# Optimization experiments

Measured on AMD Instinct MI355X. Metric: run time of the kernel, lower is better.

The kernel has to match this reference:

```python
import jax, jax.numpy as jnp
import numpy as np

# Model constants matching init_kwargs
C1, C2, FS, IMG = 1024, 3, 16, 128
NF = FS * FS                     # n_features = 256 (== pos_out_dim)
L = C1 // NF                     # 4 hypernetwork-generated layers
WD = NF + (L - 1) * NF + L       # weight_dim = 1028
M = NF // 4                      # 64 frequencies per coord dim
SIGMA = 10.0
B = 8


def _coords_pe(b):
    """get_coords([IMG, IMG]) + positional_encoding, flattened to [b, IMG*IMG, NF]."""
    v0, v1 = -0.99999, 1.0
    r = (v1 - v0) / (2 * IMG)
    seq = v0 + r + 2 * r * jnp.arange(IMG, dtype=jnp.float32)
    gy, gx = jnp.meshgrid(seq, seq, indexing='ij')
    coords = jnp.stack([gy, gx], axis=-1)                 # [IMG, IMG, 2]
    j = jnp.arange(M, dtype=jnp.float32)
    coeffs = 2.0 * jnp.pi * (SIGMA ** (j / M))            # [M]
    vp = coeffs * coords[..., None]                       # [IMG, IMG, 2, M]
    pe = jnp.concatenate([jnp.cos(vp), jnp.sin(vp)], -1)  # [IMG, IMG, 2, 2M]
    pe = pe.reshape(IMG, IMG, 4 * M)                      # flatten(-2,-1)
    x2 = pe.reshape(1, IMG * IMG, NF)
    return jnp.broadcast_to(x2, (b, IMG * IMG, NF))


def setup_inputs() -> dict:
    key = jax.random.key(0)
    ks = jax.random.split(key, 5)
    std = 0.001  # matches _initialize_weights
    x = jax.random.normal(ks[0], (B, C1, FS, FS), jnp.float32)
    conv_w = std * jax.random.normal(ks[1], (C1 + L, C1), jnp.float32)  # 1x1 conv kernel
    conv_b = jnp.zeros((C1 + L,), jnp.float32)
    wfine_w = std * jax.random.normal(ks[2], (NF, NF), jnp.float32)
    wfine_b = jnp.zeros((NF,), jnp.float32)
    last1_w = std * jax.random.normal(ks[3], (C2, NF), jnp.float32)
    last1_b = jnp.zeros((C2,), jnp.float32)
    prelu_a = jnp.array(0.25, jnp.float32)  # nn.PReLU default single param
    return {"x": x, "conv_w": conv_w, "conv_b": conv_b,
            "wfine_w": wfine_w, "wfine_b": wfine_b,
            "last1_w": last1_w, "last1_b": last1_b, "prelu_a": prelu_a}


def reference(x, conv_w, conv_b, wfine_w, wfine_b, last1_w, last1_b, prelu_a):
    b = x.shape[0]
    x2 = _coords_pe(b)  # [b, N_px, NF]
    # 1x1 conv == channel matmul
    x1 = jnp.einsum('bchw,oc->bohw', x, conv_w) + conv_b[None, :, None, None]
    W = x1.reshape(b, WD, NF)
    W = jnp.einsum('bik,jk->bij', W, wfine_w) + wfine_b  # W_fine linear
    out = x2
    for j in range(L):
        wj = W[:, NF * j + j: NF * (j + 1) + j, :]           # [b, NF, NF]
        bj = W[:, NF * (j + 1) + j: NF * (j + 1) + j + 1, :]  # [b, 1, NF]
        h = jnp.einsum('bij,bjk->bik', out, wj) + bj
        out = jnp.where(h >= 0, h, prelu_a * h)              # PReLU
    out = jnp.einsum('bik,ck->bic', out, last1_w) + last1_b  # last1
    out = jax.nn.silu(out)                                   # SiLU
    out = out.transpose(0, 2, 1).reshape(b, C2, IMG, IMG)
    return out
```

## Files before the change

kernel.cpp:

```cpp
#include <hip/hip_runtime.h>
#include <hip/hip_fp16.h>
#include <math.h>

typedef _Float16 f16;
typedef _Float16 f16x4 __attribute__((ext_vector_type(4)));
typedef _Float16 f16x8 __attribute__((ext_vector_type(8)));
typedef float f32x4 __attribute__((ext_vector_type(4)));

#define MFMA16(a, b, c) __builtin_amdgcn_mfma_f32_16x16x32_f16((a), (b), (c), 0, 0, 0)

static constexpr float SW_W    = 1024.f;
static constexpr float SA_A    = 64.f;
static constexpr float INV_SW  = 1.f / 1024.f;
static constexpr float INV_SW2 = 1.f / (1024.f * 1024.f);
static constexpr float INV_SASW = 1.f / (64.f * 1024.f);

static constexpr size_t OFF_CY = 0;
static constexpr size_t OFF_CX = OFF_CY + 65536;
static constexpr size_t OFF_LW = OFF_CX + 65536;
static constexpr size_t OFF_S  = OFF_LW + 8192;
static constexpr size_t OFF_CW = OFF_S  + 1024;
static constexpr size_t OFF_WF = OFF_CW + (size_t)1088 * 1024 * 2;
static constexpr size_t OFF_M2 = OFF_WF + 131072;
static constexpr size_t OFF_W  = OFF_M2 + (size_t)8 * 256 * 1024 * 2;
static constexpr size_t OFF_AY = OFF_W  + (size_t)8 * 1028 * 256 * 4;
static constexpr size_t OFF_BX = OFF_AY + (size_t)8 * 128 * 256 * 2;
static constexpr size_t OFF_WT = OFF_BX + (size_t)8 * 128 * 256 * 2;

static __device__ inline f32x4 zero4() { f32x4 v = {0.f, 0.f, 0.f, 0.f}; return v; }

__global__ void k_prep(float* __restrict__ cy, float* __restrict__ cx,
                       f16* __restrict__ lwf, const float* __restrict__ lw,
                       const float* __restrict__ cw, f16* __restrict__ cw16,
                       const float* __restrict__ wf, f16* __restrict__ wf16,
                       float* __restrict__ S)
{
    const int bid = blockIdx.x;
    const int t = threadIdx.x;
    if (bid < 130) {
        int id = bid * 256 + t;
        const float r = 1.99999f / 256.f;
        if (id < 32768) {
            float* dst = (id < 16384) ? cy : cx;
            int e = id & 16383;
            int row = e >> 7, f = e & 127;
            float s = -0.99999f + r + 2.f * r * (float)row;
            float coef = 6.283185307179586f * powf(10.f, (float)(f & 63) * (1.f / 64.f));
            float arg = coef * s;
            dst[e] = (f < 64) ? cosf(arg) : sinf(arg);
        } else {
            int id2 = id - 32768;
            int c = id2 >> 6, lane = id2 & 63;
            int nlo = lane & 15, q4 = lane >> 4;
            f16x8 v;
            #pragma unroll
            for (int ko = 0; ko < 8; ko++)
                v[ko] = (nlo < 3) ? (f16)(lw[nlo * 256 + (c << 5) + (q4 << 3) + ko] * SW_W) : (f16)0.f;
            *(f16x8*)(lwf + id2 * 8) = v;
        }
        return;
    }
    if (bid < 674) {
        const int g8 = (bid - 130) * 256 + t;
        const int row = g8 >> 7, col0 = (g8 & 127) << 3;
        f16x8 v;
        if (row < 1028) {
            const float* src = cw + (size_t)row * 1024 + col0;
            #pragma unroll
            for (int i = 0; i < 8; i++) v[i] = (f16)(src[i] * SW_W);
        } else {
            #pragma unroll
            for (int i = 0; i < 8; i++) v[i] = (f16)0.f;
        }
        *(f16x8*)(cw16 + (size_t)g8 * 8) = v;
        return;
    }
    if (bid < 706) {
        const int gg = (bid - 674) * 256 + t;
        const int row = gg >> 5, col0 = (gg & 31) << 3;
        const float* src = wf + (size_t)row * 256 + col0;
        f16x8 v;
        #pragma unroll
        for (int i = 0; i < 8; i++) v[i] = (f16)(src[i] * SW_W);
        *(f16x8*)(wf16 + (size_t)gg * 8) = v;
        return;
    }
    {
        const float* src = wf + (size_t)t * 256;
        float s = 0.f;
        for (int k = 0; k < 256; k++) s += src[k];
        S[t] = s;
    }
}

__global__ __launch_bounds__(256, 4) void k_gemmA(
    const float* __restrict__ x, const f16* __restrict__ wf16,
    f16* __restrict__ M2)
{
    __shared__ __align__(16) f16 Ab[2][64 * 32];
    __shared__ __align__(16) f16 Bb[2][64 * 32];
    const int t = threadIdx.x;
    const int lane = t & 63;
    const int wc = t >> 6;
    const int nlo = lane & 15, q4 = lane >> 4;
    const int blk = blockIdx.x;
    const int b = blk >> 6, rem = blk & 63;
    const int jt = rem >> 4, ct = rem & 15;
    const int j0 = jt << 6, c0 = ct << 6;

    auto stageA = [&](int buf, int k0) {
        const float* src = x + (((size_t)((b << 10) + c0 + (t >> 2))) << 8) + k0 + ((t & 3) << 3);
        f16x8 v;
        #pragma unroll
        for (int i = 0; i < 8; i++) v[i] = (f16)src[i];
        *(f16x8*)(&Ab[buf][t << 3]) = v;
    };
    auto stageB = [&](int buf, int k0) {
        *(f16x8*)(&Bb[buf][t << 3]) =
            *(const f16x8*)(wf16 + (((size_t)(j0 + (t >> 2))) << 8) + k0 + ((t & 3) << 3));
    };

    f32x4 acc[4];
    #pragma unroll
    for (int mt = 0; mt < 4; mt++) acc[mt] = zero4();

    stageA(0, 0); stageB(0, 0);
    __syncthreads();
    for (int c = 0; c < 8; c++) {
        const int cb = c & 1;
        if (c + 1 < 8) { stageA(cb ^ 1, (c + 1) << 5); stageB(cb ^ 1, (c + 1) << 5); }
        f16x8 af[4], bf;
        bf = *(const f16x8*)(&Bb[cb][(((wc << 4) + nlo) << 5) + (q4 << 3)]);
        #pragma unroll
        for (int mt = 0; mt < 4; mt++)
            af[mt] = *(const f16x8*)(&Ab[cb][(((mt << 4) + nlo) << 5) + (q4 << 3)]);
        #pragma unroll
        for (int mt = 0; mt < 4; mt++)
            acc[mt] = MFMA16(af[mt], bf, acc[mt]);
        __syncthreads();
    }
    const int j = j0 + (wc << 4) + nlo;
    #pragma unroll
    for (int mt = 0; mt < 4; mt++) {
        const int cc = c0 + (mt << 4) + (q4 << 2);
        f16x4 pk;
        #pragma unroll
        for (int i = 0; i < 4; i++) pk[i] = (f16)acc[mt][i];
        *(f16x4*)(M2 + (((size_t)((b << 8) + j)) << 10) + cc) = pk;
    }
}

__global__ __launch_bounds__(256, 4) void k_gemmB(
    const f16* __restrict__ cw16, const f16* __restrict__ M2,
    const float* __restrict__ conv_b, const float* __restrict__ S,
    const float* __restrict__ wfine_b, float* __restrict__ W)
{
    __shared__ __align__(16) f16 Ab[2][64 * 32];
    __shared__ __align__(16) f16 Bb[2][64 * 32];
    const int t = threadIdx.x;
    const int lane = t & 63;
    const int wc = t >> 6;
    const int nlo = lane & 15, q4 = lane >> 4;
    const int blk = blockIdx.x;
    const int b = blk / 68, rem = blk % 68;
    const int it = rem >> 2, jt = rem & 3;
    const int i0 = it << 6, j0 = jt << 6;

    auto stageA = [&](int buf, int k0) {
        *(f16x8*)(&Ab[buf][t << 3]) =
            *(const f16x8*)(M2 + (((size_t)((b << 8) + j0 + (t >> 2))) << 10) + k0 + ((t & 3) << 3));
    };
    auto stageB = [&](int buf, int k0) {
        *(f16x8*)(&Bb[buf][t << 3]) =
            *(const f16x8*)(cw16 + (((size_t)(i0 + (t >> 2))) << 10) + k0 + ((t & 3) << 3));
    };

    f32x4 acc[4];
    #pragma unroll
    for (int mt = 0; mt < 4; mt++) acc[mt] = zero4();

    stageA(0, 0); stageB(0, 0);
    __syncthreads();
    for (int c = 0; c < 32; c++) {
        const int cb = c & 1;
        if (c + 1 < 32) { stageA(cb ^ 1, (c + 1) << 5); stageB(cb ^ 1, (c + 1) << 5); }
        f16x8 af[4], bf;
        bf = *(const f16x8*)(&Bb[cb][(((wc << 4) + nlo) << 5) + (q4 << 3)]);
        #pragma unroll
        for (int mt = 0; mt < 4; mt++)
            af[mt] = *(const f16x8*)(&Ab[cb][(((mt << 4) + nlo) << 5) + (q4 << 3)]);
        #pragma unroll
        for (int mt = 0; mt < 4; mt++)
            acc[mt] = MFMA16(af[mt], bf, acc[mt]);
        __syncthreads();
    }
    const int i = i0 + (wc << 4) + nlo;
    if (i < 1028) {
        const float cbv = conv_b[i];
        #pragma unroll
        for (int mt = 0; mt < 4; mt++) {
            const int j = j0 + (mt << 4) + (q4 << 2);
            const f32x4 sv = *(const f32x4*)(S + j);
            const f32x4 wb = *(const f32x4*)(wfine_b + j);
            f32x4 o;
            #pragma unroll
            for (int ii = 0; ii < 4; ii++)
                o[ii] = acc[mt][ii] * INV_SW2 + cbv * sv[ii] + wb[ii];
            *(f32x4*)(W + (((size_t)(b * 1028 + i)) << 8) + j) = o;
        }
    }
}

__global__ void k_wprep(const float* __restrict__ cy, const float* __restrict__ cx,
                        const float* __restrict__ W, f16* __restrict__ ayF,
                        f16* __restrict__ bxF, f16* __restrict__ wjT)
{
    __shared__ float tile[64][65];
    const int bid = blockIdx.x;
    const int t = threadIdx.x;
    if (bid < 256) {
        const int b = bid >> 5, which = (bid >> 4) & 1, rtile = bid & 15;
        const int r0 = rtile << 3;
        const float* ctab = which ? cx : cy;
        const float* Wb = W + (size_t)(b * 1028 + (which ? 128 : 0)) * 256;
        float acc[8];
        #pragma unroll
        for (int r = 0; r < 8; r++) acc[r] = 0.f;
        for (int k = 0; k < 128; k++) {
            const float wv = Wb[(k << 8) + t];
            #pragma unroll
            for (int r = 0; r < 8; r++)
                acc[r] = fmaf(ctab[((r0 + r) << 7) + k], wv, acc[r]);
        }
        const float b1v = which ? 0.f : W[(size_t)(b * 1028 + 256) * 256 + t];
        f16* dst = which ? bxF : ayF;
        for (int r = 0; r < 8; r++)
            dst[(size_t)((b << 7) + r0 + r) * 256 + t] = (f16)((acc[r] + b1v) * SA_A);
        return;
    }
    const int id = bid - 256;
    const int b = id / 48;
    const int rr = id % 48;
    const int jj = rr / 16;
    const int tt = rr % 16;
    const int kt = tt >> 2, wt = tt & 3;
    const int k0 = kt << 6, n0 = wt << 6;
    const float* src = W + (size_t)(b * 1028 + 257 * (jj + 1)) * 256;
    for (int i = 0; i < 16; i++) {
        int e = i * 256 + t;
        int kk = e >> 6, nn = e & 63;
        tile[kk][nn] = src[(size_t)(k0 + kk) * 256 + n0 + nn];
    }
    __syncthreads();
    f16* dst = wjT + (size_t)(b * 3 + jj) * 65536;
    #pragma unroll
    for (int i = 0; i < 2; i++) {
        const int g = i * 256 + t;
        const int c_rel = g >> 8, sub = g & 255;
        const int nt = sub >> 6, ln = sub & 63;
        const int nl = ln & 15, q4g = ln >> 4;
        f16x8 v;
        #pragma unroll
        for (int ko = 0; ko < 8; ko++)
            v[ko] = (f16)(tile[(c_rel << 5) + (q4g << 3) + ko][(nt << 4) + nl] * SW_W);
        const int c = (kt << 1) + c_rel;
        *(f16x8*)(dst + (size_t)(((((c << 2) | wt) << 2) | nt) << 9) + (ln << 3)) = v;
    }
}

__global__ __launch_bounds__(256, 3) void k_main(
    const f16* __restrict__ wjT, const float* __restrict__ Wfull,
    const f16* __restrict__ ayF, const f16* __restrict__ bxF,
    const f16* __restrict__ lwf, const float* __restrict__ lb,
    const float* __restrict__ pa_p, float* __restrict__ out)
{
    __shared__ __align__(16) unsigned char actS[32768];
    const int t = threadIdx.x;
    const int lane = t & 63;
    const int wc = t >> 6;
    const int nlo = lane & 15, q4 = lane >> 4;
    const int blk = blockIdx.x;
    const int b = blk & 7, rt = blk >> 3;
    const int p0 = rt << 6;
    const int y = p0 >> 7, x0 = p0 & 127;
    const float pa = pa_p[0];

    const f16* wl0 = wjT + (size_t)(b * 3) * 65536;
    auto loadBg = [&](f16x8* dstv, int g) {
        const f16* p = wl0 + (size_t)(g >> 3) * 65536 + ((size_t)((((g & 7) << 2) | wc)) << 11) + (lane << 3);
        #pragma unroll
        for (int nt = 0; nt < 4; nt++) dstv[nt] = *(const f16x8*)(p + (nt << 9));
    };
    auto readAf = [&](f16x8* dstv, int c) {
        const int sl = (c << 2) + q4;
        #pragma unroll
        for (int pt = 0; pt < 4; pt++) {
            const int rr = (pt << 4) + nlo;
            dstv[pt] = *(const f16x8*)(actS + (rr << 9) + ((sl ^ (rr & 7)) << 4));
        }
    };
    auto lbar = [&]() {
        asm volatile("s_waitcnt lgkmcnt(0)" ::: "memory");
        __builtin_amdgcn_s_barrier();
        __builtin_amdgcn_sched_barrier(0);
    };

    f16x8 bw[3][4];
    loadBg(bw[0], 0);
    loadBg(bw[1], 1);

    {
        const int r = t & 63, g8 = t >> 6;
        const f16* ayr = ayF + (size_t)((b << 7) + y) * 256;
        const f16* bxr = bxF + (size_t)((b << 7) + x0 + r) * 256;
        const int rx = r & 7;
        #pragma unroll
        for (int mm = 0; mm < 8; mm++) {
            const int slot = (g8 << 3) + mm;
            const int f0 = slot << 3;
            f16x8 av = *(const f16x8*)(ayr + f0);
            f16x8 bv = *(const f16x8*)(bxr + f0);
            f16x8 v;
            #pragma unroll
            for (int i = 0; i < 8; i++) {
                float hv = (float)av[i] + (float)bv[i];
                hv = fmaxf(hv, 0.f) + pa * fminf(hv, 0.f);
                v[i] = (f16)hv;
            }
            *(f16x8*)(actS + (r << 9) + ((slot ^ rx) << 4)) = v;
        }
    }
    lbar();

    #pragma unroll
    for (int jj = 0; jj < 3; jj++) {
        const float* bias = Wfull + (size_t)(b * 1028 + 257 * (jj + 1) + 256) * 256;
        f32x4 bias4[4];
        #pragma unroll
        for (int nt = 0; nt < 4; nt++) {
            bias4[nt] = *(const f32x4*)(bias + (wc << 6) + (nt << 4) + (q4 << 2));
            bias4[nt] *= SA_A;
        }

        f32x4 acc[4][4];
        #pragma unroll
        for (int pt = 0; pt < 4; pt++)
            #pragma unroll
            for (int nt = 0; nt < 4; nt++) acc[pt][nt] = zero4();

        #pragma unroll
        for (int c = 0; c < 8; c++) {
            const int g = jj * 8 + c;
            f16x8* curW = bw[g % 3];
            if (g + 2 < 24) loadBg(bw[(g + 2) % 3], g + 2);
            f16x8 af[4];
            readAf(af, c);
            __builtin_amdgcn_s_setprio(1);
            #pragma unroll
            for (int pt = 0; pt < 4; pt++)
                #pragma unroll
                for (int nt = 0; nt < 4; nt++)
                    acc[pt][nt] = MFMA16(curW[nt], af[pt], acc[pt][nt]);
            __builtin_amdgcn_s_setprio(0);
        }
        lbar();

        #pragma unroll
        for (int nt = 0; nt < 4; nt++) {
            const int nb = (wc << 6) + (nt << 4) + (q4 << 2);
            #pragma unroll
            for (int pt = 0; pt < 4; pt++) {
                const int rr = (pt << 4) + nlo;
                f16x4 pk;
                #pragma unroll
                for (int i = 0; i < 4; i++) {
                    float v = fmaf(acc[pt][nt][i], INV_SW, bias4[nt][i]);
                    v = fmaxf(v, 0.f) + pa * fminf(v, 0.f);
                    pk[i] = (f16)v;
                }
                *(f16x4*)(actS + (rr << 9) + (((nb >> 3) ^ (rr & 7)) << 4) + ((nb & 7) << 1)) = pk;
            }
        }
        lbar();
    }

    {
        f32x4 acc2 = zero4();
        const int rr = (wc << 4) + nlo;
        #pragma unroll
        for (int c = 0; c < 8; c++) {
            const int sl = (c << 2) + q4;
            const f16x8 af = *(const f16x8*)(actS + (rr << 9) + ((sl ^ (rr & 7)) << 4));
            const f16x8 lf = *(const f16x8*)(lwf + (((c << 6) + lane) << 3));
            acc2 = MFMA16(af, lf, acc2);
        }
        if (nlo < 3) {
            const float lbv = lb[nlo];
            float* ob = out + ((size_t)(b * 3 + nlo) << 14) + p0 + (wc << 4) + (q4 << 2);
            #pragma unroll
            for (int i = 0; i < 4; i++) {
                float z = acc2[i] * INV_SASW + lbv;
                ob[i] = z / (1.f + expf(-z));
            }
        }
    }
}

extern "C" void kernel_launch(void* const* d_in, const int* in_sizes, int n_in,
                              void* d_out, int out_size, void* d_ws, size_t ws_size,
                              hipStream_t stream)
{
    (void)in_sizes; (void)n_in; (void)out_size; (void)ws_size;
    const float* x       = (const float*)d_in[0];
    const float* conv_w  = (const float*)d_in[1];
    const float* conv_b  = (const float*)d_in[2];
    const float* wfine_w = (const float*)d_in[3];
    const float* wfine_b = (const float*)d_in[4];
    const float* last1_w = (const float*)d_in[5];
    const float* last1_b = (const float*)d_in[6];
    const float* prelu_a = (const float*)d_in[7];
    char* ws = (char*)d_ws;
    float* Cy  = (float*)(ws + OFF_CY);
    float* Cx  = (float*)(ws + OFF_CX);
    f16*   lwf = (f16*)(ws + OFF_LW);
    float* S   = (float*)(ws + OFF_S);
    f16*   cw16= (f16*)(ws + OFF_CW);
    f16*   wf16= (f16*)(ws + OFF_WF);
    f16*   M2  = (f16*)(ws + OFF_M2);
    float* W   = (float*)(ws + OFF_W);
    f16*   AyF = (f16*)(ws + OFF_AY);
    f16*   BxF = (f16*)(ws + OFF_BX);
    f16*   wjT = (f16*)(ws + OFF_WT);

    k_prep<<<707, 256, 0, stream>>>(Cy, Cx, lwf, last1_w, conv_w, cw16, wfine_w, wf16, S);
    k_gemmA<<<512, 256, 0, stream>>>(x, wf16, M2);
    k_gemmB<<<544, 256, 0, stream>>>(cw16, M2, conv_b, S, wfine_b, W);
    k_wprep<<<640, 256, 0, stream>>>(Cy, Cx, W, AyF, BxF, wjT);
    k_main<<<2048, 256, 0, stream>>>(wjT, W, AyF, BxF, lwf, last1_b, prelu_a, (float*)d_out);
}
```

Before: 133.9 us.

## Merge prep and first GEMM into one launch; simplify main-kernel weight prefetch

The separate prep and gemmA kernels become one kernel whose blocks split by index. The fp16 wfine conversion is done inline while staging the GEMM B tile, so the wf16 buffer and one launch go away. The row-sum loop is vectorised. In the main kernel, triple-buffered weight prefetch becomes double buffering, the outer jj loop is no longer unrolled, and the setprio hints are removed, which lowers register pressure but shortens the prefetch distance.

```diff
diff --git a/kernel.cpp b/kernel.cpp
--- a/kernel.cpp
+++ b/kernel.cpp
@@ -20,8 +20,7 @@
 static constexpr size_t OFF_LW = OFF_CX + 65536;
 static constexpr size_t OFF_S  = OFF_LW + 8192;
 static constexpr size_t OFF_CW = OFF_S  + 1024;
-static constexpr size_t OFF_WF = OFF_CW + (size_t)1088 * 1024 * 2;
-static constexpr size_t OFF_M2 = OFF_WF + 131072;
+static constexpr size_t OFF_M2 = OFF_CW + (size_t)1088 * 1024 * 2;
 static constexpr size_t OFF_W  = OFF_M2 + (size_t)8 * 256 * 1024 * 2;
 static constexpr size_t OFF_AY = OFF_W  + (size_t)8 * 1028 * 256 * 4;
 static constexpr size_t OFF_BX = OFF_AY + (size_t)8 * 128 * 256 * 2;
@@ -29,16 +28,73 @@
 
 static __device__ inline f32x4 zero4() { f32x4 v = {0.f, 0.f, 0.f, 0.f}; return v; }
 
-__global__ void k_prep(float* __restrict__ cy, float* __restrict__ cx,
-                       f16* __restrict__ lwf, const float* __restrict__ lw,
-                       const float* __restrict__ cw, f16* __restrict__ cw16,
-                       const float* __restrict__ wf, f16* __restrict__ wf16,
-                       float* __restrict__ S)
+__global__ __launch_bounds__(256, 4) void k_prepA(
+    const float* __restrict__ x, const float* __restrict__ wfine,
+    f16* __restrict__ M2,
+    float* __restrict__ cy, float* __restrict__ cx,
+    f16* __restrict__ lwf, const float* __restrict__ lw,
+    const float* __restrict__ cw, f16* __restrict__ cw16,
+    float* __restrict__ S)
 {
+    __shared__ __align__(16) f16 Ab[2][64 * 32];
+    __shared__ __align__(16) f16 Bb[2][64 * 32];
     const int bid = blockIdx.x;
     const int t = threadIdx.x;
-    if (bid < 130) {
-        int id = bid * 256 + t;
+    if (bid < 512) {
+        const int lane = t & 63;
+        const int wc = t >> 6;
+        const int nlo = lane & 15, q4 = lane >> 4;
+        const int b = bid >> 6, rem = bid & 63;
+        const int jt = rem >> 4, ct = rem & 15;
+        const int j0 = jt << 6, c0 = ct << 6;
+
+        auto stageA = [&](int buf, int k0) {
+            const float* src = x + (((size_t)((b << 10) + c0 + (t >> 2))) << 8) + k0 + ((t & 3) << 3);
+            f16x8 v;
+            #pragma unroll
+            for (int i = 0; i < 8; i++) v[i] = (f16)src[i];
+            *(f16x8*)(&Ab[buf][t << 3]) = v;
+        };
+        auto stageB = [&](int buf, int k0) {
+            const float* src = wfine + (size_t)(j0 + (t >> 2)) * 256 + k0 + ((t & 3) << 3);
+            f16x8 v;
+            #pragma unroll
+            for (int i = 0; i < 8; i++) v[i] = (f16)(src[i] * SW_W);
+            *(f16x8*)(&Bb[buf][t << 3]) = v;
+        };
+
+        f32x4 acc[4];
+        #pragma unroll
+        for (int mt = 0; mt < 4; mt++) acc[mt] = zero4();
+
+        stageA(0, 0); stageB(0, 0);
+        __syncthreads();
+        for (int c = 0; c < 8; c++) {
+            const int cb = c & 1;
+            if (c + 1 < 8) { stageA(cb ^ 1, (c + 1) << 5); stageB(cb ^ 1, (c + 1) << 5); }
+            f16x8 af[4], bf;
+            bf = *(const f16x8*)(&Bb[cb][(((wc << 4) + nlo) << 5) + (q4 << 3)]);
+            #pragma unroll
+            for (int mt = 0; mt < 4; mt++)
+                af[mt] = *(const f16x8*)(&Ab[cb][(((mt << 4) + nlo) << 5) + (q4 << 3)]);
+            #pragma unroll
+            for (int mt = 0; mt < 4; mt++)
+                acc[mt] = MFMA16(af[mt], bf, acc[mt]);
+            __syncthreads();
+        }
+        const int j = j0 + (wc << 4) + nlo;
+        #pragma unroll
+        for (int mt = 0; mt < 4; mt++) {
+            const int cc = c0 + (mt << 4) + (q4 << 2);
+            f16x4 pk;
+            #pragma unroll
+            for (int i = 0; i < 4; i++) pk[i] = (f16)acc[mt][i];
+            *(f16x4*)(M2 + (((size_t)((b << 8) + j)) << 10) + cc) = pk;
+        }
+        return;
+    }
+    if (bid < 642) {
+        int id = (bid - 512) * 256 + t;
         const float r = 1.99999f / 256.f;
         if (id < 32768) {
             float* dst = (id < 16384) ? cy : cx;
@@ -60,8 +116,8 @@
         }
         return;
     }
-    if (bid < 674) {
-        const int g8 = (bid - 130) * 256 + t;
+    if (bid < 1186) {
+        const int g8 = (bid - 642) * 256 + t;
         const int row = g8 >> 7, col0 = (g8 & 127) << 3;
         f16x8 v;
         if (row < 1028) {
@@ -75,78 +131,14 @@
         *(f16x8*)(cw16 + (size_t)g8 * 8) = v;
         return;
     }
-    if (bid < 706) {
-        const int gg = (bid - 674) * 256 + t;
-        const int row = gg >> 5, col0 = (gg & 31) << 3;
-        const float* src = wf + (size_t)row * 256 + col0;
-        f16x8 v;
-        #pragma unroll
-        for (int i = 0; i < 8; i++) v[i] = (f16)(src[i] * SW_W);
-        *(f16x8*)(wf16 + (size_t)gg * 8) = v;
-        return;
-    }
     {
-        const float* src = wf + (size_t)t * 256;
+        const float* src = wfine + (size_t)t * 256;
         float s = 0.f;
-        for (int k = 0; k < 256; k++) s += src[k];
+        for (int k = 0; k < 256; k += 4) {
+            const f32x4 v = *(const f32x4*)(src + k);
+            s += (v[0] + v[1]) + (v[2] + v[3]);
+        }
         S[t] = s;
-    }
-}
-
-__global__ __launch_bounds__(256, 4) void k_gemmA(
-    const float* __restrict__ x, const f16* __restrict__ wf16,
-    f16* __restrict__ M2)
-{
-    __shared__ __align__(16) f16 Ab[2][64 * 32];
-    __shared__ __align__(16) f16 Bb[2][64 * 32];
-    const int t = threadIdx.x;
-    const int lane = t & 63;
-    const int wc = t >> 6;
-    const int nlo = lane & 15, q4 = lane >> 4;
-    const int blk = blockIdx.x;
-    const int b = blk >> 6, rem = blk & 63;
-    const int jt = rem >> 4, ct = rem & 15;
-    const int j0 = jt << 6, c0 = ct << 6;
-
-    auto stageA = [&](int buf, int k0) {
-        const float* src = x + (((size_t)((b << 10) + c0 + (t >> 2))) << 8) + k0 + ((t & 3) << 3);
-        f16x8 v;
-        #pragma unroll
-        for (int i = 0; i < 8; i++) v[i] = (f16)src[i];
-        *(f16x8*)(&Ab[buf][t << 3]) = v;
-    };
-    auto stageB = [&](int buf, int k0) {
-        *(f16x8*)(&Bb[buf][t << 3]) =
-            *(const f16x8*)(wf16 + (((size_t)(j0 + (t >> 2))) << 8) + k0 + ((t & 3) << 3));
-    };
-
-    f32x4 acc[4];
-    #pragma unroll
-    for (int mt = 0; mt < 4; mt++) acc[mt] = zero4();
-
-    stageA(0, 0); stageB(0, 0);
-    __syncthreads();
-    for (int c = 0; c < 8; c++) {
-        const int cb = c & 1;
-        if (c + 1 < 8) { stageA(cb ^ 1, (c + 1) << 5); stageB(cb ^ 1, (c + 1) << 5); }
-        f16x8 af[4], bf;
-        bf = *(const f16x8*)(&Bb[cb][(((wc << 4) + nlo) << 5) + (q4 << 3)]);
-        #pragma unroll
-        for (int mt = 0; mt < 4; mt++)
-            af[mt] = *(const f16x8*)(&Ab[cb][(((mt << 4) + nlo) << 5) + (q4 << 3)]);
-        #pragma unroll
-        for (int mt = 0; mt < 4; mt++)
-            acc[mt] = MFMA16(af[mt], bf, acc[mt]);
-        __syncthreads();
-    }
-    const int j = j0 + (wc << 4) + nlo;
-    #pragma unroll
-    for (int mt = 0; mt < 4; mt++) {
-        const int cc = c0 + (mt << 4) + (q4 << 2);
-        f16x4 pk;
-        #pragma unroll
-        for (int i = 0; i < 4; i++) pk[i] = (f16)acc[mt][i];
-        *(f16x4*)(M2 + (((size_t)((b << 8) + j)) << 10) + cc) = pk;
     }
 }
 
@@ -291,23 +283,14 @@
         #pragma unroll
         for (int nt = 0; nt < 4; nt++) dstv[nt] = *(const f16x8*)(p + (nt << 9));
     };
-    auto readAf = [&](f16x8* dstv, int c) {
-        const int sl = (c << 2) + q4;
-        #pragma unroll
-        for (int pt = 0; pt < 4; pt++) {
-            const int rr = (pt << 4) + nlo;
-            dstv[pt] = *(const f16x8*)(actS + (rr << 9) + ((sl ^ (rr & 7)) << 4));
-        }
-    };
     auto lbar = [&]() {
         asm volatile("s_waitcnt lgkmcnt(0)" ::: "memory");
         __builtin_amdgcn_s_barrier();
         __builtin_amdgcn_sched_barrier(0);
     };
 
-    f16x8 bw[3][4];
-    loadBg(bw[0], 0);
-    loadBg(bw[1], 1);
+    f16x8 bfA[4], bfB[4];
+    loadBg(bfA, 0);
 
     {
         const int r = t & 63, g8 = t >> 6;
@@ -332,7 +315,6 @@
     }
     lbar();
 
-    #pragma unroll
     for (int jj = 0; jj < 3; jj++) {
         const float* bias = Wfull + (size_t)(b * 1028 + 257 * (jj + 1) + 256) * 256;
         f32x4 bias4[4];
@@ -351,17 +333,21 @@
         #pragma unroll
         for (int c = 0; c < 8; c++) {
             const int g = jj * 8 + c;
-            f16x8* curW = bw[g % 3];
-            if (g + 2 < 24) loadBg(bw[(g + 2) % 3], g + 2);
+            f16x8* curW = (c & 1) ? bfB : bfA;
+            f16x8* nxtW = (c & 1) ? bfA : bfB;
+            if (g < 23) loadBg(nxtW, g + 1);
+            const int sl = (c << 2) + q4;
             f16x8 af[4];
-            readAf(af, c);
-            __builtin_amdgcn_s_setprio(1);
+            #pragma unroll
+            for (int pt = 0; pt < 4; pt++) {
+                const int rr = (pt << 4) + nlo;
+                af[pt] = *(const f16x8*)(actS + (rr << 9) + ((sl ^ (rr & 7)) << 4));
+            }
             #pragma unroll
             for (int pt = 0; pt < 4; pt++)
                 #pragma unroll
                 for (int nt = 0; nt < 4; nt++)
                     acc[pt][nt] = MFMA16(curW[nt], af[pt], acc[pt][nt]);
-            __builtin_amdgcn_s_setprio(0);
         }
         lbar();
 
@@ -425,15 +411,13 @@
     f16*   lwf = (f16*)(ws + OFF_LW);
     float* S   = (float*)(ws + OFF_S);
     f16*   cw16= (f16*)(ws + OFF_CW);
-    f16*   wf16= (f16*)(ws + OFF_WF);
     f16*   M2  = (f16*)(ws + OFF_M2);
     float* W   = (float*)(ws + OFF_W);
     f16*   AyF = (f16*)(ws + OFF_AY);
     f16*   BxF = (f16*)(ws + OFF_BX);
     f16*   wjT = (f16*)(ws + OFF_WT);
 
-    k_prep<<<707, 256, 0, stream>>>(Cy, Cx, lwf, last1_w, conv_w, cw16, wfine_w, wf16, S);
-    k_gemmA<<<512, 256, 0, stream>>>(x, wf16, M2);
+    k_prepA<<<1187, 256, 0, stream>>>(x, wfine_w, M2, Cy, Cx, lwf, last1_w, conv_w, cw16, S);
     k_gemmB<<<544, 256, 0, stream>>>(cw16, M2, conv_b, S, wfine_b, W);
     k_wprep<<<640, 256, 0, stream>>>(Cy, Cx, W, AyF, BxF, wjT);
     k_main<<<2048, 256, 0, stream>>>(wjT, W, AyF, BxF, lwf, last1_b, prelu_a, (float*)d_out);
```

Measured after the change: 113.3 us. 15.4% less time.
